# Kernel tuning notes

Measured on AMD Instinct MI355X. Metric: run time of the kernel, lower is better.

Reference implementation:

```python
import jax, jax.numpy as jnp
import numpy as np

NUM_HEADS = 16
NUM_KV_HEADS = 4
HEAD_DIM = 64
ROPE_BASE = 10000.0


def _rope(x, pos0):
    # x: [b, s, n, h_d]; interleaved-pair RoPE (torchtune RotaryPositionalEmbeddings)
    b, s, n, hd = x.shape
    half = hd // 2
    inv_freq = 1.0 / (ROPE_BASE ** (jnp.arange(0, hd, 2, dtype=jnp.float32) / hd))  # [half]
    t = jnp.arange(s, dtype=jnp.float32) + pos0                                      # [s]
    freqs = t[:, None] * inv_freq[None, :]                                           # [s, half]
    cos = jnp.cos(freqs)[None, :, None, :].astype(x.dtype)
    sin = jnp.sin(freqs)[None, :, None, :].astype(x.dtype)
    xr = x.reshape(b, s, n, half, 2)
    x1, x2 = xr[..., 0], xr[..., 1]
    o1 = x1 * cos - x2 * sin
    o2 = x1 * sin + x2 * cos
    return jnp.stack([o1, o2], axis=-1).reshape(b, s, n, hd)


def setup_inputs() -> dict:
    key = jax.random.key(0)
    k1, k2, k3 = jax.random.split(key, 3)
    b, s, d = 2, 2048, 1024
    qkv_dim = (NUM_HEADS + 2 * NUM_KV_HEADS) * HEAD_DIM  # 1536
    x = jax.random.normal(k1, (b, s, d), dtype=jnp.float32)
    Wqkv = jax.random.normal(k2, (d, qkv_dim), dtype=jnp.float32) * (d ** -0.5)
    Wo = jax.random.normal(k3, (d, d), dtype=jnp.float32) * (d ** -0.5)
    return {"x": x, "Wqkv": Wqkv, "Wo": Wo, "curr_pos": 0}


def reference(x, Wqkv, Wo, curr_pos):
    b, s, d = x.shape
    n_h, n_kv, hd = NUM_HEADS, NUM_KV_HEADS, HEAD_DIM
    q_per_kv = n_h // n_kv
    total_qkv = q_per_kv + 2

    # fused QKV projection then split per kv group
    qkv = (x @ Wqkv).reshape(b, s, n_kv, total_qkv, hd)
    q = qkv[:, :, :, :q_per_kv]            # [b, s, n_kv, q_per_kv, hd]
    k = qkv[:, :, :, q_per_kv:q_per_kv + 1]  # [b, s, n_kv, 1, hd]
    v = qkv[:, :, :, q_per_kv + 1:]          # [b, s, n_kv, 1, hd]

    # GQA expand k/v to match query heads, then flatten heads
    k = jnp.broadcast_to(k, (b, s, n_kv, q_per_kv, hd))
    v = jnp.broadcast_to(v, (b, s, n_kv, q_per_kv, hd))
    q = q.reshape(b, s, n_h, hd)
    k = k.reshape(b, s, n_h, hd)
    v = v.reshape(b, s, n_h, hd)

    # RoPE on q and k
    q = _rope(q, curr_pos)
    k = _rope(k, curr_pos)

    # causal SDPA (kv_cache is None -> is_causal=True, mask=None, dropout=0)
    scale = 1.0 / jnp.sqrt(jnp.asarray(hd, dtype=x.dtype))
    scores = jnp.einsum('bqhd,bkhd->bhqk', q, k) * scale  # [b, n_h, s, s]
    causal = jnp.tril(jnp.ones((s, s), dtype=bool))
    scores = jnp.where(causal[None, None], scores, jnp.finfo(scores.dtype).min)
    attn = jax.nn.softmax(scores, axis=-1)
    out = jnp.einsum('bhqk,bkhd->bqhd', attn, v).reshape(b, s, n_h * hd)
    return out @ Wo
```

## Files before the change

kernel.cpp:

```cpp
#include <hip/hip_runtime.h>
#include <hip/hip_bf16.h>

typedef __attribute__((ext_vector_type(8))) short bf16x8;
typedef __attribute__((ext_vector_type(4))) short bf16x4;
typedef __attribute__((ext_vector_type(4))) float f32x4;
typedef unsigned short u16;
typedef unsigned int u32;

#define NH 16
#define NKV 4
#define HD 64
#define BB 2
#define SS 2048
#define DD 1024
#define QKVD 1536

#define QSCALE 0.18033688011112f
#define MBIAS  -12.0f

template<bool B> struct BoolC { static constexpr bool value = B; };
template<int V>  struct IntC  { static constexpr int value = V; };

__device__ __forceinline__ u16 f2b(float f){
  __hip_bfloat16 h = __float2bfloat16(f);
  u16 u; __builtin_memcpy(&u, &h, 2); return u;
}
__device__ __forceinline__ float b2f(u32 u){
  u <<= 16; float f; __builtin_memcpy(&f, &u, 4); return f;
}
__device__ __forceinline__ float exp2fast(float x){
#if __has_builtin(__builtin_amdgcn_exp2f)
  return __builtin_amdgcn_exp2f(x);
#else
  return exp2f(x);
#endif
}

__device__ __forceinline__ void gload16(const void* g, void* l){
  __builtin_amdgcn_global_load_lds((const __attribute__((address_space(1))) void*)g,
                                   (__attribute__((address_space(3))) void*)l, 16, 0, 0);
}

__device__ __forceinline__ f32x4 mfma16(bf16x4 a, bf16x4 b, f32x4 c){
#if __has_builtin(__builtin_amdgcn_mfma_f32_16x16x16bf16_1k)
  return __builtin_amdgcn_mfma_f32_16x16x16bf16_1k(a, b, c, 0, 0, 0);
#else
  asm volatile("v_mfma_f32_16x16x16_bf16 %0, %1, %2, %0" : "+v"(c) : "v"(a), "v"(b));
  return c;
#endif
}

__global__ __launch_bounds__(256) void prep1(const float* __restrict__ x,
                                             u16* __restrict__ Xb,
                                             const float* __restrict__ Wqkv,
                                             u16* __restrict__ WqkvT,
                                             const float* __restrict__ Wo,
                                             u16* __restrict__ WoT){
  __shared__ u16 tile[64][65];
  const int bid = blockIdx.x;
  if (bid < 4096){
    int idx = (bid * 256 + threadIdx.x) * 4;
    float4 v = *(const float4*)(x + idx);
    u32 lo = (u32)f2b(v.x) | ((u32)f2b(v.y) << 16);
    u32 hi = (u32)f2b(v.z) | ((u32)f2b(v.w) << 16);
    *(uint2*)(Xb + idx) = make_uint2(lo, hi);
    return;
  }
  const float* in; u16* outT; int K, N, n0, k0;
  if (bid < 4480){
    int id = bid - 4096; in = Wqkv; outT = WqkvT; K = 1024; N = 1536;
    n0 = (id % 24) * 64; k0 = (id / 24) * 64;
  } else {
    int id = bid - 4480; in = Wo; outT = WoT; K = 1024; N = 1024;
    n0 = (id % 16) * 64; k0 = (id / 16) * 64;
  }
  int cr = threadIdx.x >> 6, cc = threadIdx.x & 63;
#pragma unroll
  for (int rr = 0; rr < 16; rr++){
    int row = rr * 4 + cr;
    tile[row][cc] = f2b(in[(size_t)(k0 + row) * N + n0 + cc]);
  }
  __syncthreads();
#pragma unroll
  for (int rr = 0; rr < 16; rr++){
    int row = rr * 4 + cr;
    outT[(size_t)(n0 + row) * K + k0 + cc] = tile[cc][row];
  }
}

template<int TN, typename OT>
__global__ __launch_bounds__(256) void gemm_db(const __hip_bfloat16* __restrict__ A,
                                               const __hip_bfloat16* __restrict__ BT,
                                               OT* __restrict__ C,
                                               int M, int N, int K){
  constexpr int NW = TN / 32;
  constexpr int ABYTES = 128 * 128;
  constexpr int BBYTES = TN * 128;
  __shared__ __align__(16) char smem[2][ABYTES + BBYTES];
  const int ntn = N / TN;
  int bid = blockIdx.x;
  const int cpx = gridDim.x >> 3;
  bid = (bid & 7) * cpx + (bid >> 3);
  const int tm = bid / ntn, tn = bid % ntn;
  const int m0 = tm << 7, n0 = tn * TN;
  const int lane = threadIdx.x & 63, w = threadIdx.x >> 6;
  const int g = lane >> 4, i = lane & 15;
  const int wr = w >> 1, wc = w & 1;
  f32x4 acc[4][NW] = {};
  const int lrow = lane >> 3;
  const int lcol = ((lane & 7) ^ lrow) * 8;
  const __hip_bfloat16* ga = A  + (size_t)(m0 + w * 32 + lrow) * K + lcol;
  const __hip_bfloat16* gb = BT + (size_t)(n0 + w * 8 + lrow) * K + lcol;
  const int xr = (i & 7) << 4;

  auto stage = [&](int buf, int kt){
    char* As = smem[buf];
    char* Bs = As + ABYTES;
#pragma unroll
    for (int h = 0; h < 4; h++)
      gload16(ga + kt + (size_t)(h * 8) * K, As + w * 4096 + h * 1024);
#pragma unroll
    for (int h = 0; h < NW; h++)
      gload16(gb + kt + (size_t)(h * 32) * K, Bs + (h * 4 + w) * 1024);
  };

  stage(0, 0);
  asm volatile("s_waitcnt vmcnt(0)");
  __syncthreads();
  int cur = 0;
  for (int kt = 0; kt < K; kt += 64){
    if (kt + 64 < K) stage(cur ^ 1, kt + 64);
    const char* As = smem[cur];
    const char* Bs = As + ABYTES;
    bf16x8 af[2][4], bfr[2][NW];
#pragma unroll
    for (int kh = 0; kh < 2; kh++){
#pragma unroll
      for (int x = 0; x < 4; x++)
        af[kh][x] = *(const bf16x8*)(As + (wr * 64 + x * 16 + i) * 128 + ((kh * 64 + g * 16) ^ xr));
#pragma unroll
      for (int n = 0; n < NW; n++)
        bfr[kh][n] = *(const bf16x8*)(Bs + (wc * (TN / 2) + n * 16 + i) * 128 + ((kh * 64 + g * 16) ^ xr));
    }
    __builtin_amdgcn_s_setprio(1);
#pragma unroll
    for (int kh = 0; kh < 2; kh++)
#pragma unroll
      for (int mi = 0; mi < 4; mi++)
#pragma unroll
        for (int ni = 0; ni < NW; ni++)
          acc[mi][ni] = __builtin_amdgcn_mfma_f32_16x16x32_bf16(af[kh][mi], bfr[kh][ni], acc[mi][ni], 0, 0, 0);
    __builtin_amdgcn_s_setprio(0);
    asm volatile("s_waitcnt vmcnt(0)");
    __syncthreads();
    cur ^= 1;
  }
#pragma unroll
  for (int mi = 0; mi < 4; mi++)
#pragma unroll
    for (int ni = 0; ni < NW; ni++){
      size_t base = (size_t)(m0 + wr * 64 + mi * 16 + g * 4) * N + n0 + wc * (TN / 2) + ni * 16 + i;
#pragma unroll
      for (int r = 0; r < 4; r++){
        float v = acc[mi][ni][r];
        if constexpr (sizeof(OT) == 2) C[base + (size_t)r * N] = (OT)f2b(v);
        else                           C[base + (size_t)r * N] = v;
      }
    }
}

__global__ __launch_bounds__(256) void prep2(const u16* __restrict__ qkv,
                                             const int* __restrict__ posp,
                                             u16* __restrict__ Qr,
                                             u16* __restrict__ Kr,
                                             u16* __restrict__ Vt){
  __shared__ u16 tile[64][65];
  const int bid = blockIdx.x;
  if (bid < 10240){
    int bx = bid & 255, h20 = (bid >> 8) % 20, bi = bid / 5120;
    int t = bx * 256 + threadIdx.x;
    int p = t & 31, si = t >> 5;
    int kvh = h20 / 5, slot = h20 - kvh * 5;
    const u16* src = qkv + (size_t)(bi * SS + si) * QKVD + (kvh * 6 + slot) * 64 + 2 * p;
    u32 pair = *(const u32*)src;
    float x1 = b2f(pair & 0xffffu), x2 = b2f(pair >> 16);
    int pos0 = posp[0];
    float inv_freq = exp2fast(-(float)p * 0.4152410118609203f);
    float ang = (float)(si + pos0) * inv_freq;
    float sn, cs;
    sincosf(ang, &sn, &cs);
    float o1 = x1 * cs - x2 * sn;
    float o2 = x1 * sn + x2 * cs;
    u16* dst;
    if (slot == 4){
      dst = Kr + ((size_t)(bi * NKV + kvh) * SS + si) * 64 + 2 * p;
    } else {
      o1 *= QSCALE; o2 *= QSCALE;
      dst = Qr + ((size_t)(bi * NH + kvh * 4 + slot) * SS + si) * 64 + 2 * p;
    }
    *(u32*)dst = (u32)f2b(o1) | ((u32)f2b(o2) << 16);
    return;
  }
  int id2 = bid - 10240;
  int st0 = (id2 & 31) * 64;
  int bkv = id2 >> 5;
  int bi = bkv >> 2, kvh = bkv & 3;
  int cr = threadIdx.x >> 6, cc = threadIdx.x & 63;
  const u16* src = qkv + (size_t)(bi * SS + st0) * QKVD + (kvh * 6 + 5) * 64;
#pragma unroll
  for (int rr = 0; rr < 16; rr++){
    int row = rr * 4 + cr;
    tile[row][cc] = src[(size_t)row * QKVD + cc];
  }
  __syncthreads();
  u16* dst = Vt + (size_t)bkv * 64 * SS + st0;
#pragma unroll
  for (int rr = 0; rr < 16; rr++){
    int row = rr * 4 + cr;
    dst[(size_t)row * SS + cc] = tile[cc][row];
  }
}

__global__ __launch_bounds__(512) void attn_fwd(const __hip_bfloat16* __restrict__ Qr,
                                                const __hip_bfloat16* __restrict__ Kr,
                                                const __hip_bfloat16* __restrict__ Vt,
                                                u16* __restrict__ Ao){
  __shared__ __align__(16) char smem[32768];
  const int blk = blockIdx.x;
  const int qt = 15 - (blk >> 5);
  const int bh = blk & 31;
  const int hi = bh & 15;
  const int bi = bh >> 4;
  const int kvh = hi >> 2;
  const int tid = threadIdx.x;
  const int lane = tid & 63, w = tid >> 6;
  const int g = lane >> 4, i = lane & 15;
  const int q0 = qt * 128 + w * 16;
  const u16* Qp = (const u16*)Qr + (size_t)(bi * NH + hi) * SS * 64;
  const u16* Kp = (const u16*)Kr + (size_t)(bi * NKV + kvh) * SS * 64;
  const u16* Vp = (const u16*)Vt + (size_t)(bi * NKV + kvh) * 64 * SS;
  bf16x8 qf0 = *(const bf16x8*)(Qp + (size_t)(q0 + i) * 64 + g * 8);
  bf16x8 qf1 = *(const bf16x8*)(Qp + (size_t)(q0 + i) * 64 + 32 + g * 8);

  const int srow = tid >> 3;
  const int sw   = ((tid & 7) ^ (srow & 7)) * 8;
  const int xr   = (i & 7) << 4;

  auto stage = [&](int buf, int j0){
    gload16(Kp + (size_t)(j0 + srow) * 64 + sw, &smem[buf * 16384 + w * 1024]);
    gload16(Vp + (size_t)srow * SS + j0 + sw,   &smem[buf * 16384 + 8192 + w * 1024]);
  };

  float l_row = 0.f;
  f32x4 o[4] = {};
  const int wlim = w * 16 + i;

  auto body = [&](auto modec, int buf){
    constexpr int MODE = decltype(modec)::value;
    if constexpr (MODE == 2){ if (w < 4) return; }
    const char* Kb = &smem[buf * 16384];
    const char* Vb = Kb + 8192;
    f32x4 st[4];
    __builtin_amdgcn_s_setprio(1);
#pragma unroll
    for (int jb = 0; jb < 4; jb++){
      const int row = jb * 16 + i;
      bf16x8 kf0 = *(const bf16x8*)(Kb + row * 128 + ((g * 16) ^ xr));
      bf16x8 kf1 = *(const bf16x8*)(Kb + row * 128 + ((64 + g * 16) ^ xr));
      f32x4 a = {MBIAS, MBIAS, MBIAS, MBIAS};
      a = __builtin_amdgcn_mfma_f32_16x16x32_bf16(kf0, qf0, a, 0, 0, 0);
      a = __builtin_amdgcn_mfma_f32_16x16x32_bf16(kf1, qf1, a, 0, 0, 0);
      st[jb] = a;
    }
    __builtin_amdgcn_s_setprio(0);
    bf16x4 vt[4][4];
#pragma unroll
    for (int db = 0; db < 4; db++){
      const int row = db * 16 + i;
#pragma unroll
      for (int mk = 0; mk < 4; mk++)
        vt[db][mk] = *(const bf16x4*)(Vb + row * 128 + ((mk * 32 + g * 8) ^ xr));
    }
    auto smpv = [&](auto diagc, int wl){
      constexpr bool DIAG = decltype(diagc)::value;
      float p[4][4];
#pragma unroll
      for (int jb = 0; jb < 4; jb++)
#pragma unroll
        for (int r = 0; r < 4; r++){
          float e = exp2fast(st[jb][r]);
          if constexpr (DIAG) e = (jb * 16 + g * 4 + r > wl) ? 0.f : e;
          p[jb][r] = e;
        }
      float sj[4];
#pragma unroll
      for (int jb = 0; jb < 4; jb++)
        sj[jb] = (p[jb][0] + p[jb][1]) + (p[jb][2] + p[jb][3]);
      float lsum = (sj[0] + sj[1]) + (sj[2] + sj[3]);
      lsum += __shfl_xor(lsum, 16, 64);
      lsum += __shfl_xor(lsum, 32, 64);
      l_row += lsum;
      __builtin_amdgcn_s_setprio(1);
#pragma unroll
      for (int mk = 0; mk < 4; mk++){
        bf16x4 pa;
#pragma unroll
        for (int r = 0; r < 4; r++) pa[r] = (short)f2b(p[mk][r]);
#pragma unroll
        for (int db = 0; db < 4; db++)
          o[db] = mfma16(vt[db][mk], pa, o[db]);
      }
      __builtin_amdgcn_s_setprio(0);
    };
    if constexpr (MODE == 0){
      smpv(BoolC<false>{}, 0);
    } else if constexpr (MODE == 1){
      if (w < 4) smpv(BoolC<true>{}, wlim);
      else       smpv(BoolC<false>{}, 0);
    } else {
      smpv(BoolC<true>{}, wlim - 64);
    }
  };

  stage(0, 0);
  asm volatile("s_waitcnt vmcnt(0)");
  __syncthreads();
  int cur = 0;
  const int nfull = 2 * qt;
  for (int kt = 0; kt < nfull; kt++){
    stage(cur ^ 1, (kt + 1) * 64);
    body(IntC<0>{}, cur);
    asm volatile("s_waitcnt vmcnt(0)");
    __syncthreads();
    cur ^= 1;
  }
  stage(cur ^ 1, (nfull + 1) * 64);
  body(IntC<1>{}, cur);
  asm volatile("s_waitcnt vmcnt(0)");
  __syncthreads();
  cur ^= 1;
  body(IntC<2>{}, cur);

  const float linv = 1.f / l_row;
  u16* orow = Ao + (size_t)(bi * SS + q0 + i) * (NH * HD) + hi * 64 + g * 4;
#pragma unroll
  for (int db = 0; db < 4; db++){
    bf16x4 ov;
#pragma unroll
    for (int r = 0; r < 4; r++) ov[r] = (short)f2b(o[db][r] * linv);
    *(bf16x4*)(orow + db * 16) = ov;
  }
}

extern "C" void kernel_launch(void* const* d_in, const int* in_sizes, int n_in,
                              void* d_out, int out_size, void* d_ws, size_t ws_size,
                              hipStream_t stream){
  const float* x    = (const float*)d_in[0];
  const float* Wqkv = (const float*)d_in[1];
  const float* Wo   = (const float*)d_in[2];
  const int*   pos  = (const int*)d_in[3];
  float* out = (float*)d_out;
  char* ws = (char*)d_ws;

  __hip_bfloat16* Xb    = (__hip_bfloat16*)(ws);
  __hip_bfloat16* WqkvT = (__hip_bfloat16*)(ws + 8388608);
  __hip_bfloat16* WoT   = (__hip_bfloat16*)(ws + 11534336);
  u16*            QKVb  = (u16*)(ws + 13631488);
  __hip_bfloat16* Qr    = (__hip_bfloat16*)(ws + 26214400);
  __hip_bfloat16* Kr    = (__hip_bfloat16*)(ws + 34603008);
  __hip_bfloat16* Vt    = (__hip_bfloat16*)(ws + 36700160);
  __hip_bfloat16* Ao    = (__hip_bfloat16*)(ws);

  prep1<<<4736, 256, 0, stream>>>(x, (u16*)Xb, Wqkv, (u16*)WqkvT, Wo, (u16*)WoT);
  gemm_db<96, u16><<<512, 256, 0, stream>>>(Xb, WqkvT, QKVb, 4096, 1536, 1024);
  prep2<<<10496, 256, 0, stream>>>(QKVb, pos, (u16*)Qr, (u16*)Kr, (u16*)Vt);
  attn_fwd<<<512, 512, 0, stream>>>(Qr, Kr, Vt, (u16*)Ao);
  gemm_db<64, float><<<512, 256, 0, stream>>>(Ao, WoT, out, 4096, 1024, 1024);
}
```

Measured before the change: 91.47 us.

## Triple-buffer K/V tiles in attention with partial vmcnt waits

Moves the attention kernel's K/V shared-memory staging from double to triple buffering. Loads now run two tiles ahead, and each iteration waits only for the older tile (vmcnt(2)) before a single barrier, instead of draining all loads. This should hide global-load latency better and removes one barrier per iteration. In exchange, LDS use rises to 48KB per block, which may lower occupancy. The vmcnt(2) count also assumes each stage issues exactly two vector loads per thread.

New measurement: 92.30 us. No clear change (+0.9%).

```diff
diff --git a/kernel.cpp b/kernel.cpp
--- a/kernel.cpp
+++ b/kernel.cpp
@@ -225,7 +225,7 @@
                                                 const __hip_bfloat16* __restrict__ Kr,
                                                 const __hip_bfloat16* __restrict__ Vt,
                                                 u16* __restrict__ Ao){
-  __shared__ __align__(16) char smem[32768];
+  __shared__ __align__(16) char smem[3 * 16384];
   const int blk = blockIdx.x;
   const int qt = 15 - (blk >> 5);
   const int bh = blk & 31;
@@ -322,24 +322,24 @@
     }
   };
 
+  const int nfull = 2 * qt;
   stage(0, 0);
-  asm volatile("s_waitcnt vmcnt(0)");
-  __syncthreads();
-  int cur = 0;
-  const int nfull = 2 * qt;
-  for (int kt = 0; kt < nfull; kt++){
-    stage(cur ^ 1, (kt + 1) * 64);
-    body(IntC<0>{}, cur);
-    asm volatile("s_waitcnt vmcnt(0)");
-    __syncthreads();
-    cur ^= 1;
-  }
-  stage(cur ^ 1, (nfull + 1) * 64);
-  body(IntC<1>{}, cur);
-  asm volatile("s_waitcnt vmcnt(0)");
-  __syncthreads();
-  cur ^= 1;
-  body(IntC<2>{}, cur);
+  stage(1, 64);
+  for (int t = 0; t < nfull; t++){
+    asm volatile("s_waitcnt vmcnt(2)" ::: "memory");
+    __builtin_amdgcn_s_barrier();
+    asm volatile("" ::: "memory");
+    stage((t + 2) % 3, (t + 2) * 64);
+    body(IntC<0>{}, t % 3);
+  }
+  asm volatile("s_waitcnt vmcnt(2)" ::: "memory");
+  __builtin_amdgcn_s_barrier();
+  asm volatile("" ::: "memory");
+  body(IntC<1>{}, nfull % 3);
+  asm volatile("s_waitcnt vmcnt(0)" ::: "memory");
+  __builtin_amdgcn_s_barrier();
+  asm volatile("" ::: "memory");
+  body(IntC<2>{}, (nfull + 1) % 3);
 
   const float linv = 1.f / l_row;
   u16* orow = Ao + (size_t)(bi * SS + q0 + i) * (NH * HD) + hi * 64 + g * 4;
```

## Switch attention to 32x32x16 MFMA with 4 waves of 32 query rows

Applied to the files above, without the earlier changes.

The attention kernel now uses 32x32x16 bf16 MFMA for both QK^T and PV instead of 16x16 tiles, with each of 4 waves owning 32 query rows, so blocks drop from 512 to 256 threads. P is packed to bf16 with v_cvt_pk_bf16_f32 and rearranged across half-waves with v_permlane32_swap so it can feed the PV MFMA directly from registers without going through LDS. Causal masking now uses absolute key and query indices. The larger MFMA shape reduces instruction count and raises per-wave work, at the cost of more registers per wave, fewer waves per block, and gfx950-specific inline assembly.

Measured after the change: 84.21 us. 1.09x faster.

```diff
diff --git a/kernel.cpp b/kernel.cpp
--- a/kernel.cpp
+++ b/kernel.cpp
@@ -4,6 +4,7 @@
 typedef __attribute__((ext_vector_type(8))) short bf16x8;
 typedef __attribute__((ext_vector_type(4))) short bf16x4;
 typedef __attribute__((ext_vector_type(4))) float f32x4;
+typedef __attribute__((ext_vector_type(16))) float f32x16;
 typedef unsigned short u16;
 typedef unsigned int u32;
 
@@ -18,8 +19,7 @@
 #define QSCALE 0.18033688011112f
 #define MBIAS  -12.0f
 
-template<bool B> struct BoolC { static constexpr bool value = B; };
-template<int V>  struct IntC  { static constexpr int value = V; };
+template<int V> struct IntC { static constexpr int value = V; };
 
 __device__ __forceinline__ u16 f2b(float f){
   __hip_bfloat16 h = __float2bfloat16(f);
@@ -39,15 +39,6 @@
 __device__ __forceinline__ void gload16(const void* g, void* l){
   __builtin_amdgcn_global_load_lds((const __attribute__((address_space(1))) void*)g,
                                    (__attribute__((address_space(3))) void*)l, 16, 0, 0);
-}
-
-__device__ __forceinline__ f32x4 mfma16(bf16x4 a, bf16x4 b, f32x4 c){
-#if __has_builtin(__builtin_amdgcn_mfma_f32_16x16x16bf16_1k)
-  return __builtin_amdgcn_mfma_f32_16x16x16bf16_1k(a, b, c, 0, 0, 0);
-#else
-  asm volatile("v_mfma_f32_16x16x16_bf16 %0, %1, %2, %0" : "+v"(c) : "v"(a), "v"(b));
-  return c;
-#endif
 }
 
 __global__ __launch_bounds__(256) void prep1(const float* __restrict__ x,
@@ -221,11 +212,11 @@
   }
 }
 
-__global__ __launch_bounds__(512) void attn_fwd(const __hip_bfloat16* __restrict__ Qr,
+__global__ __launch_bounds__(256) void attn_fwd(const __hip_bfloat16* __restrict__ Qr,
                                                 const __hip_bfloat16* __restrict__ Kr,
                                                 const __hip_bfloat16* __restrict__ Vt,
                                                 u16* __restrict__ Ao){
-  __shared__ __align__(16) char smem[32768];
+  __shared__ __align__(16) char smem[2][16384];
   const int blk = blockIdx.x;
   const int qt = 15 - (blk >> 5);
   const int bh = blk & 31;
@@ -234,92 +225,100 @@
   const int kvh = hi >> 2;
   const int tid = threadIdx.x;
   const int lane = tid & 63, w = tid >> 6;
-  const int g = lane >> 4, i = lane & 15;
-  const int q0 = qt * 128 + w * 16;
+  const int qr = lane & 31, hlf = lane >> 5;
+  const int q0 = qt * 128 + w * 32;
+  const int qabs = q0 + qr;
   const u16* Qp = (const u16*)Qr + (size_t)(bi * NH + hi) * SS * 64;
   const u16* Kp = (const u16*)Kr + (size_t)(bi * NKV + kvh) * SS * 64;
   const u16* Vp = (const u16*)Vt + (size_t)(bi * NKV + kvh) * 64 * SS;
-  bf16x8 qf0 = *(const bf16x8*)(Qp + (size_t)(q0 + i) * 64 + g * 8);
-  bf16x8 qf1 = *(const bf16x8*)(Qp + (size_t)(q0 + i) * 64 + 32 + g * 8);
+
+  bf16x8 qb[4];
+#pragma unroll
+  for (int ks = 0; ks < 4; ks++)
+    qb[ks] = *(const bf16x8*)(Qp + (size_t)(q0 + qr) * 64 + ks * 16 + hlf * 8);
 
   const int srow = tid >> 3;
   const int sw   = ((tid & 7) ^ (srow & 7)) * 8;
-  const int xr   = (i & 7) << 4;
+  const int xr   = (lane & 7) << 4;
 
   auto stage = [&](int buf, int j0){
-    gload16(Kp + (size_t)(j0 + srow) * 64 + sw, &smem[buf * 16384 + w * 1024]);
-    gload16(Vp + (size_t)srow * SS + j0 + sw,   &smem[buf * 16384 + 8192 + w * 1024]);
+#pragma unroll
+    for (int n = 0; n < 2; n++)
+      gload16(Kp + (size_t)(j0 + n * 32 + srow) * 64 + sw,
+              &smem[buf][n * 4096 + tid * 16]);
+#pragma unroll
+    for (int n = 0; n < 2; n++)
+      gload16(Vp + (size_t)(n * 32 + srow) * SS + j0 + sw,
+              &smem[buf][8192 + n * 4096 + tid * 16]);
   };
 
   float l_row = 0.f;
-  f32x4 o[4] = {};
-  const int wlim = w * 16 + i;
-
-  auto body = [&](auto modec, int buf){
+  f32x16 o[2] = {};
+
+  auto body = [&](auto modec, int buf, int j0){
     constexpr int MODE = decltype(modec)::value;
-    if constexpr (MODE == 2){ if (w < 4) return; }
-    const char* Kb = &smem[buf * 16384];
+    if constexpr (MODE == 2){ if (w < 2) return; }
+    const bool msk = (MODE == 1) ? (w < 2) : (MODE == 2);
+    const char* Kb = smem[buf];
     const char* Vb = Kb + 8192;
-    f32x4 st[4];
+    f32x16 st[2];
     __builtin_amdgcn_s_setprio(1);
 #pragma unroll
-    for (int jb = 0; jb < 4; jb++){
-      const int row = jb * 16 + i;
-      bf16x8 kf0 = *(const bf16x8*)(Kb + row * 128 + ((g * 16) ^ xr));
-      bf16x8 kf1 = *(const bf16x8*)(Kb + row * 128 + ((64 + g * 16) ^ xr));
-      f32x4 a = {MBIAS, MBIAS, MBIAS, MBIAS};
-      a = __builtin_amdgcn_mfma_f32_16x16x32_bf16(kf0, qf0, a, 0, 0, 0);
-      a = __builtin_amdgcn_mfma_f32_16x16x32_bf16(kf1, qf1, a, 0, 0, 0);
+    for (int jb = 0; jb < 2; jb++){
+      f32x16 a = {MBIAS, MBIAS, MBIAS, MBIAS, MBIAS, MBIAS, MBIAS, MBIAS,
+                  MBIAS, MBIAS, MBIAS, MBIAS, MBIAS, MBIAS, MBIAS, MBIAS};
+      const int row = jb * 32 + qr;
+#pragma unroll
+      for (int ks = 0; ks < 4; ks++){
+        bf16x8 kf = *(const bf16x8*)(Kb + row * 128 + ((ks * 32 + hlf * 16) ^ xr));
+        a = __builtin_amdgcn_mfma_f32_32x32x16_bf16(kf, qb[ks], a, 0, 0, 0);
+      }
       st[jb] = a;
     }
     __builtin_amdgcn_s_setprio(0);
-    bf16x4 vt[4][4];
-#pragma unroll
-    for (int db = 0; db < 4; db++){
-      const int row = db * 16 + i;
-#pragma unroll
-      for (int mk = 0; mk < 4; mk++)
-        vt[db][mk] = *(const bf16x4*)(Vb + row * 128 + ((mk * 32 + g * 8) ^ xr));
-    }
-    auto smpv = [&](auto diagc, int wl){
-      constexpr bool DIAG = decltype(diagc)::value;
-      float p[4][4];
-#pragma unroll
-      for (int jb = 0; jb < 4; jb++)
-#pragma unroll
-        for (int r = 0; r < 4; r++){
-          float e = exp2fast(st[jb][r]);
-          if constexpr (DIAG) e = (jb * 16 + g * 4 + r > wl) ? 0.f : e;
-          p[jb][r] = e;
+    bf16x8 vA[2][4];
+#pragma unroll
+    for (int db = 0; db < 2; db++){
+      const int row = db * 32 + qr;
+#pragma unroll
+      for (int ks = 0; ks < 4; ks++)
+        vA[db][ks] = *(const bf16x8*)(Vb + row * 128 + ((ks * 32 + hlf * 16) ^ xr));
+    }
+    float lsum = 0.f;
+#pragma unroll
+    for (int jb = 0; jb < 2; jb++){
+      float p[16];
+#pragma unroll
+      for (int r = 0; r < 16; r++){
+        float e = exp2fast(st[jb][r]);
+        if (msk){
+          int jabs = j0 + jb * 32 + (r & 3) + 8 * (r >> 2) + 4 * hlf;
+          e = (jabs > qabs) ? 0.f : e;
         }
-      float sj[4];
-#pragma unroll
-      for (int jb = 0; jb < 4; jb++)
-        sj[jb] = (p[jb][0] + p[jb][1]) + (p[jb][2] + p[jb][3]);
-      float lsum = (sj[0] + sj[1]) + (sj[2] + sj[3]);
-      lsum += __shfl_xor(lsum, 16, 64);
-      lsum += __shfl_xor(lsum, 32, 64);
-      l_row += lsum;
+        p[r] = e;
+        lsum += e;
+      }
+      u32 c[8];
+#pragma unroll
+      for (int m = 0; m < 8; m++)
+        asm("v_cvt_pk_bf16_f32 %0, %1, %2" : "=v"(c[m]) : "v"(p[2 * m]), "v"(p[2 * m + 1]));
+      asm volatile("v_permlane32_swap_b32 %0, %1" : "+v"(c[0]), "+v"(c[2]));
+      asm volatile("v_permlane32_swap_b32 %0, %1" : "+v"(c[1]), "+v"(c[3]));
+      asm volatile("v_permlane32_swap_b32 %0, %1" : "+v"(c[4]), "+v"(c[6]));
+      asm volatile("v_permlane32_swap_b32 %0, %1" : "+v"(c[5]), "+v"(c[7]));
+      bf16x8 pfE, pfO;
+      __builtin_memcpy(&pfE, &c[0], 16);
+      __builtin_memcpy(&pfO, &c[4], 16);
       __builtin_amdgcn_s_setprio(1);
 #pragma unroll
-      for (int mk = 0; mk < 4; mk++){
-        bf16x4 pa;
-#pragma unroll
-        for (int r = 0; r < 4; r++) pa[r] = (short)f2b(p[mk][r]);
-#pragma unroll
-        for (int db = 0; db < 4; db++)
-          o[db] = mfma16(vt[db][mk], pa, o[db]);
+      for (int db = 0; db < 2; db++){
+        o[db] = __builtin_amdgcn_mfma_f32_32x32x16_bf16(vA[db][jb * 2 + 0], pfE, o[db], 0, 0, 0);
+        o[db] = __builtin_amdgcn_mfma_f32_32x32x16_bf16(vA[db][jb * 2 + 1], pfO, o[db], 0, 0, 0);
       }
       __builtin_amdgcn_s_setprio(0);
-    };
-    if constexpr (MODE == 0){
-      smpv(BoolC<false>{}, 0);
-    } else if constexpr (MODE == 1){
-      if (w < 4) smpv(BoolC<true>{}, wlim);
-      else       smpv(BoolC<false>{}, 0);
-    } else {
-      smpv(BoolC<true>{}, wlim - 64);
-    }
+    }
+    lsum += __shfl_xor(lsum, 32, 64);
+    l_row += lsum;
   };
 
   stage(0, 0);
@@ -327,29 +326,31 @@
   __syncthreads();
   int cur = 0;
   const int nfull = 2 * qt;
-  for (int kt = 0; kt < nfull; kt++){
-    stage(cur ^ 1, (kt + 1) * 64);
-    body(IntC<0>{}, cur);
+  for (int t = 0; t < nfull; t++){
+    stage(cur ^ 1, (t + 1) * 64);
+    body(IntC<0>{}, cur, t * 64);
     asm volatile("s_waitcnt vmcnt(0)");
     __syncthreads();
     cur ^= 1;
   }
   stage(cur ^ 1, (nfull + 1) * 64);
-  body(IntC<1>{}, cur);
+  body(IntC<1>{}, cur, nfull * 64);
   asm volatile("s_waitcnt vmcnt(0)");
   __syncthreads();
   cur ^= 1;
-  body(IntC<2>{}, cur);
+  body(IntC<2>{}, cur, (nfull + 1) * 64);
 
   const float linv = 1.f / l_row;
-  u16* orow = Ao + (size_t)(bi * SS + q0 + i) * (NH * HD) + hi * 64 + g * 4;
-#pragma unroll
-  for (int db = 0; db < 4; db++){
-    bf16x4 ov;
-#pragma unroll
-    for (int r = 0; r < 4; r++) ov[r] = (short)f2b(o[db][r] * linv);
-    *(bf16x4*)(orow + db * 16) = ov;
-  }
+  u16* orow = Ao + (size_t)(bi * SS + q0 + qr) * (NH * HD) + hi * 64 + hlf * 4;
+#pragma unroll
+  for (int db = 0; db < 2; db++)
+#pragma unroll
+    for (int tg = 0; tg < 4; tg++){
+      bf16x4 ov;
+#pragma unroll
+      for (int r = 0; r < 4; r++) ov[r] = (short)f2b(o[db][tg * 4 + r] * linv);
+      *(bf16x4*)(orow + db * 32 + tg * 8) = ov;
+    }
 }
 
 extern "C" void kernel_launch(void* const* d_in, const int* in_sizes, int n_in,
@@ -374,6 +375,6 @@
   prep1<<<4736, 256, 0, stream>>>(x, (u16*)Xb, Wqkv, (u16*)WqkvT, Wo, (u16*)WoT);
   gemm_db<96, u16><<<512, 256, 0, stream>>>(Xb, WqkvT, QKVb, 4096, 1536, 1024);
   prep2<<<10496, 256, 0, stream>>>(QKVb, pos, (u16*)Qr, (u16*)Kr, (u16*)Vt);
-  attn_fwd<<<512, 512, 0, stream>>>(Qr, Kr, Vt, (u16*)Ao);
+  attn_fwd<<<512, 256, 0, stream>>>(Qr, Kr, Vt, (u16*)Ao);
   gemm_db<64, float><<<512, 256, 0, stream>>>(Ao, WoT, out, 4096, 1024, 1024);
 }
```
